# Optimization experiments

Measured on AMD Instinct MI355X. Metric: run time of the kernel, lower is better.

Reference implementation:

```python
import jax, jax.numpy as jnp
import numpy as np

BS, EMB, RES = 256, 768, 14
N_MASKS, HID, OUT, N_PROJ = 16, 4096, 256, 4
BN_EPS = 1e-5


def setup_inputs() -> dict:
    key = jax.random.key(0)
    ks = jax.random.split(key, 8)
    x = jax.random.normal(ks[0], (BS, EMB, RES, RES), jnp.float32)
    # binary ROI masks over the 14x14 = 196 patch grid
    masks = (jax.random.uniform(ks[1], (BS, N_MASKS, RES * RES)) < 0.3).astype(jnp.float32)
    projection_idx = jax.random.randint(ks[2], (N_MASKS,), 0, N_PROJ, jnp.int32)
    mask_ids = jax.random.randint(ks[3], (BS, N_MASKS), 0, 100, jnp.int32)
    # stacked params for the N_PROJ MLP projectors
    W1 = jax.random.normal(ks[4], (N_PROJ, EMB, HID), jnp.float32) * 0.02
    b1 = jnp.zeros((N_PROJ, HID), jnp.float32)
    gamma = jnp.ones((N_PROJ, HID), jnp.float32)
    beta = jnp.zeros((N_PROJ, HID), jnp.float32)
    W2 = jax.random.normal(ks[5], (N_PROJ, HID, OUT), jnp.float32) * 0.02
    b2 = jnp.zeros((N_PROJ, OUT), jnp.float32)
    return {"x": x, "masks": masks, "projection_idx": projection_idx,
            "mask_ids": mask_ids, "W1": W1, "b1": b1, "gamma": gamma,
            "beta": beta, "W2": W2, "b2": b2}


def reference(x, masks, projection_idx, mask_ids, W1, b1, gamma, beta, W2, b2):
    bs, emb, hx, hy = x.shape
    # [bs, emb, hx, hy] -> [bs, hw, emb]
    emb_local = jnp.transpose(x, (0, 2, 3, 1)).reshape(bs, hx * hy, emb)
    # mask-normalized pooling:  pooled[b,n,:] = mean of embeddings inside mask n
    area = masks.sum(axis=-1, keepdims=True)
    smpl = masks / jnp.maximum(area, 1.0)
    pooled = smpl @ emb_local                       # [bs, n_masks, emb]
    # dense dispatch: run EVERY projector over all pooled tokens (as original)
    h = jnp.einsum('bne,peh->pbnh', pooled, W1) + b1[:, None, None, :]
    # BatchNorm1d in training mode over flattened (bs*n_masks) batch, per projector
    mu = h.mean(axis=(1, 2), keepdims=True)
    var = jnp.mean(jnp.square(h - mu), axis=(1, 2), keepdims=True)  # biased var
    h = (h - mu) * jax.lax.rsqrt(var + BN_EPS) * gamma[:, None, None, :] + beta[:, None, None, :]
    h = jax.nn.relu(h)
    o = jnp.einsum('pbnh,pho->pbno', h, W2) + b2[:, None, None, :]   # [P, bs, n, out]
    # keep only projector projection_idx[n] for mask-slot n (disjoint selection)
    n_proj = W1.shape[0]
    sel = (projection_idx[None, :] == jnp.arange(n_proj)[:, None]).astype(o.dtype)  # [P, n]
    xs = (o * sel[:, None, :, None]).sum(axis=0)     # [bs, n_masks, out]
    return (xs, mask_ids)
```

## Files before the change

### kernel.cpp

```cpp
#include <hip/hip_runtime.h>
#include <hip/hip_bf16.h>

#define BS 256
#define EMB 768
#define HW 196
#define NMASK 16
#define HID 4096
#define OUT 256
#define NPROJ 4
#define MROWS 4096

typedef __attribute__((ext_vector_type(8))) short bf16x8;
typedef __attribute__((ext_vector_type(4))) float f32x4;
typedef __attribute__((ext_vector_type(8))) unsigned short u16x8;

__device__ inline float bf2f(unsigned short u) {
    unsigned int x = ((unsigned int)u) << 16;
    return __builtin_bit_cast(float, x);
}
__device__ inline short f2bfs(float f) {
    return __builtin_bit_cast(short, __float2bfloat16(f));
}

#define GL16(gptr, lptr)                                                     \
    __builtin_amdgcn_global_load_lds(                                        \
        (const __attribute__((address_space(1))) void*)(gptr),               \
        (__attribute__((address_space(3))) void*)(lptr), 16, 0, 0)

__global__ __launch_bounds__(256) void maskprep(
    const float* __restrict__ masks, short* __restrict__ afrG,
    float* __restrict__ invG)
{
    const int b = blockIdx.x, tid = threadIdx.x;
    const float* mb = masks + (size_t)b * NMASK * HW;
    short* ag = afrG + (size_t)b * 3584;
    for (int s = tid; s < 7 * 64; s += 256) {
        int m = s & 15, kb = ((s >> 4) & 3) * 8 + (s >> 6) * 32;
        bf16x8 v;
        #pragma unroll
        for (int j = 0; j < 8; ++j) {
            int kk = kb + j;
            v[j] = (kk < HW) ? f2bfs(mb[m * HW + kk]) : (short)0;
        }
        *(bf16x8*)(ag + s * 8) = v;
    }
    if (tid >= 192) {
        int l = tid - 192, m = l >> 2, q = l & 3;
        float a = 0.f;
        for (int hw = q; hw < HW; hw += 4) a += mb[m * HW + hw];
        a += __shfl_xor(a, 1);
        a += __shfl_xor(a, 2);
        if (q == 0) invG[b * NMASK + m] = 1.0f / fmaxf(a, 1.0f);
    }
}

__global__ __launch_bounds__(256) void pool_main(
    const float* __restrict__ x, const short* __restrict__ afrG,
    const float* __restrict__ invG, __hip_bfloat16* __restrict__ pooledG)
{
    __shared__ __align__(16) short afr[3584];
    __shared__ float inv[NMASK];
    const int bid = blockIdx.x;
    const int b = bid / 12, ec = bid % 12;
    const int tid = threadIdx.x, lane = tid & 63, w = tid >> 6;
    const int lc = lane & 15, l4 = lane >> 4;

    const int e = ec * 64 + w * 16 + lc;
    const float* xrow = x + ((size_t)b * EMB + e) * HW;
    float4 u[6][2];
    #pragma unroll
    for (int kc = 0; kc < 6; ++kc) {
        u[kc][0] = *(const float4*)(xrow + kc * 32 + l4 * 8);
        u[kc][1] = *(const float4*)(xrow + kc * 32 + l4 * 8 + 4);
    }
    float4 ut = (l4 == 0) ? *(const float4*)(xrow + 192)
                          : float4{0.f, 0.f, 0.f, 0.f};

    {
        const char* src = (const char*)(afrG + (size_t)b * 3584);
        #pragma unroll
        for (int r = 0; r < 2; ++r) {
            int cb = r * 256 + w * 64;
            if (cb < 448)
                GL16(src + (size_t)cb * 16 + (size_t)lane * 16,
                     (char*)afr + cb * 16);
        }
    }
    if (tid < NMASK) inv[tid] = invG[b * NMASK + tid];
    __syncthreads();

    const bf16x8* afv = (const bf16x8*)afr;
    f32x4 acc = {};
    #pragma unroll
    for (int kc = 0; kc < 6; ++kc) {
        bf16x8 af = afv[kc * 64 + lane];
        bf16x8 bf;
        bf[0] = f2bfs(u[kc][0].x); bf[1] = f2bfs(u[kc][0].y);
        bf[2] = f2bfs(u[kc][0].z); bf[3] = f2bfs(u[kc][0].w);
        bf[4] = f2bfs(u[kc][1].x); bf[5] = f2bfs(u[kc][1].y);
        bf[6] = f2bfs(u[kc][1].z); bf[7] = f2bfs(u[kc][1].w);
        acc = __builtin_amdgcn_mfma_f32_16x16x32_bf16(af, bf, acc, 0, 0, 0);
    }
    {
        bf16x8 af = afv[6 * 64 + lane];
        bf16x8 bf = {};
        if (l4 == 0) {
            bf[0] = f2bfs(ut.x); bf[1] = f2bfs(ut.y);
            bf[2] = f2bfs(ut.z); bf[3] = f2bfs(ut.w);
        }
        acc = __builtin_amdgcn_mfma_f32_16x16x32_bf16(af, bf, acc, 0, 0, 0);
    }

    #pragma unroll
    for (int j = 0; j < 4; ++j) {
        int m = l4 * 4 + j;
        pooledG[((size_t)m * 256 + b) * EMB + e] =
            __float2bfloat16(acc[j] * inv[m]);
    }
}

__global__ __launch_bounds__(256) void prep(
    const float* __restrict__ W1, const float* __restrict__ W2,
    const __hip_bfloat16* __restrict__ pg,
    __hip_bfloat16* __restrict__ W1T, __hip_bfloat16* __restrict__ W2T,
    __hip_bfloat16* __restrict__ pgT)
{
    __shared__ __align__(16) char sm[64 * 65 * 4];
    const int bid = blockIdx.x, tid = threadIdx.x;
    if (bid < 4096) {
        const float* src; __hip_bfloat16* dst; int R, C, x, y, z;
        if (bid < 3072) { z = bid / 768; int r = bid % 768; x = r % 64; y = r / 64;
                          src = W1; dst = W1T; R = EMB; C = HID; }
        else            { int b2 = bid - 3072; z = b2 / 256; int r = b2 % 256;
                          x = r % 4; y = r / 4; src = W2; dst = W2T; R = HID; C = OUT; }
        float (*tile)[65] = (float(*)[65])sm;
        const float* s = src + (size_t)z * R * C;
        __hip_bfloat16* d = dst + (size_t)z * R * C;
        const int c0 = x * 64, r0 = y * 64;
        for (int i = tid; i < 4096; i += 256) {
            int r = i >> 6, c = i & 63;
            tile[r][c] = s[(size_t)(r0 + r) * C + c0 + c];
        }
        __syncthreads();
        for (int i = tid; i < 4096; i += 256) {
            int c = i >> 6, r = i & 63;
            d[(size_t)(c0 + c) * R + r0 + r] = __float2bfloat16(tile[r][c]);
        }
    } else {
        const int b3 = bid - 4096;
        const int x = b3 % 12, y = b3 / 12;
        __hip_bfloat16 (*tile)[65] = (__hip_bfloat16(*)[65])sm;
        const int c0 = x * 64, r0 = y * 64;
        for (int i = tid; i < 4096; i += 256) {
            int r = i >> 6, c = i & 63;
            tile[r][c] = pg[(size_t)(r0 + r) * EMB + c0 + c];
        }
        __syncthreads();
        for (int i = tid; i < 4096; i += 256) {
            int c = i >> 6, r = i & 63;
            pgT[(size_t)(c0 + c) * MROWS + r0 + r] = tile[r][c];
        }
    }
}

__global__ __launch_bounds__(256) void meanpool(
    const __hip_bfloat16* __restrict__ PT, float* __restrict__ mp)
{
    const int e = blockIdx.x, tid = threadIdx.x;
    const u16x8* p = (const u16x8*)(PT + (size_t)e * MROWS);
    u16x8 v1 = p[tid], v2 = p[tid + 256];
    float s = 0.f;
    #pragma unroll
    for (int j = 0; j < 8; ++j) s += bf2f((unsigned short)v1[j]) + bf2f((unsigned short)v2[j]);
    #pragma unroll
    for (int o = 1; o < 64; o <<= 1) s += __shfl_xor(s, o);
    __shared__ float wsum[4];
    if ((tid & 63) == 0) wsum[tid >> 6] = s;
    __syncthreads();
    if (tid == 0) mp[e] = (wsum[0] + wsum[1] + wsum[2] + wsum[3]) * (1.0f / 4096.0f);
}

__global__ __launch_bounds__(256) void cgemm(
    const __hip_bfloat16* __restrict__ PT, float* __restrict__ Cpart)
{
    __shared__ __align__(16) __hip_bfloat16 As[128 * 32];
    __shared__ __align__(16) __hip_bfloat16 Bs[128 * 32];
    const int tid = threadIdx.x, lane = tid & 63, wid = tid >> 6;
    const int n0 = blockIdx.x * 128, m0 = blockIdx.y * 128, kbase = blockIdx.z * 512;
    float* Cp = Cpart + (size_t)blockIdx.z * EMB * EMB;
    const int wr = wid >> 1, wc = wid & 1;
    const int l4 = lane >> 4, lc = lane & 15;

    f32x4 acc[4][4] = {};
    for (int k0 = kbase; k0 < kbase + 512; k0 += 32) {
        __syncthreads();
        #pragma unroll
        for (int r = 0; r < 2; ++r) {
            int t = r * 256 + tid;
            int row = t >> 2, ko = (t & 3) * 8;
            GL16(PT + (size_t)(m0 + row) * MROWS + k0 + ko, &As[(r * 256 + wid * 64) * 8]);
        }
        #pragma unroll
        for (int r = 0; r < 2; ++r) {
            int t = r * 256 + tid;
            int row = t >> 2, ko = (t & 3) * 8;
            GL16(PT + (size_t)(n0 + row) * MROWS + k0 + ko, &Bs[(r * 256 + wid * 64) * 8]);
        }
        __syncthreads();
        const bf16x8* Av = (const bf16x8*)As;
        const bf16x8* Bv = (const bf16x8*)Bs;
        bf16x8 a[4], b[4];
        #pragma unroll
        for (int m = 0; m < 4; ++m) a[m] = Av[(wr * 64 + m * 16 + lc) * 4 + l4];
        #pragma unroll
        for (int n = 0; n < 4; ++n) b[n] = Bv[(wc * 64 + n * 16 + lc) * 4 + l4];
        #pragma unroll
        for (int m = 0; m < 4; ++m)
            #pragma unroll
            for (int n = 0; n < 4; ++n)
                acc[m][n] = __builtin_amdgcn_mfma_f32_16x16x32_bf16(a[m], b[n], acc[m][n], 0, 0, 0);
    }
    #pragma unroll
    for (int m = 0; m < 4; ++m)
        #pragma unroll
        for (int n = 0; n < 4; ++n)
            #pragma unroll
            for (int j = 0; j < 4; ++j) {
                int row = m0 + wr * 64 + m * 16 + l4 * 4 + j;
                int col = n0 + wc * 64 + n * 16 + lc;
                Cp[(size_t)row * EMB + col] = acc[m][n][j];
            }
}

__global__ __launch_bounds__(256) void cvt_c(
    const float* __restrict__ Cpart, __hip_bfloat16* __restrict__ Cbf)
{
    int i = (blockIdx.x * 256 + threadIdx.x) * 4;
    float sx = 0.f, sy = 0.f, sz = 0.f, sw = 0.f;
    #pragma unroll
    for (int kz = 0; kz < 8; ++kz) {
        float4 v = *(const float4*)(Cpart + (size_t)kz * EMB * EMB + i);
        sx += v.x; sy += v.y; sz += v.z; sw += v.w;
    }
    const float s = 1.0f / 4096.0f;
    Cbf[i + 0] = __float2bfloat16(sx * s);
    Cbf[i + 1] = __float2bfloat16(sy * s);
    Cbf[i + 2] = __float2bfloat16(sz * s);
    Cbf[i + 3] = __float2bfloat16(sw * s);
}

__global__ __launch_bounds__(256) void ugemm(
    const __hip_bfloat16* __restrict__ W1T, const __hip_bfloat16* __restrict__ Cbf,
    const float* __restrict__ mp,
    float* __restrict__ Eh2p, float* __restrict__ Mup)
{
    __shared__ __align__(16) __hip_bfloat16 As[128 * 32];
    __shared__ __align__(16) __hip_bfloat16 Bs[128 * 32];
    const int tid = threadIdx.x, lane = tid & 63, wid = tid >> 6;
    const int n0 = blockIdx.x * 128, m0 = blockIdx.y * 128, p = blockIdx.z;
    const __hip_bfloat16* Ap = W1T + (size_t)p * HID * EMB;
    const int wr = wid >> 1, wc = wid & 1;
    const int l4 = lane >> 4, lc = lane & 15;

    f32x4 acc[4][4] = {};
    for (int k0 = 0; k0 < EMB; k0 += 32) {
        __syncthreads();
        #pragma unroll
        for (int r = 0; r < 2; ++r) {
            int t = r * 256 + tid;
            int row = t >> 2, ko = (t & 3) * 8;
            GL16(Ap + (size_t)(m0 + row) * EMB + k0 + ko, &As[(r * 256 + wid * 64) * 8]);
        }
        #pragma unroll
        for (int r = 0; r < 2; ++r) {
            int t = r * 256 + tid;
            int row = t >> 2, ko = (t & 3) * 8;
            GL16(Cbf + (size_t)(n0 + row) * EMB + k0 + ko, &Bs[(r * 256 + wid * 64) * 8]);
        }
        __syncthreads();
        const bf16x8* Av = (const bf16x8*)As;
        const bf16x8* Bv = (const bf16x8*)Bs;
        bf16x8 a[4], b[4];
        #pragma unroll
        for (int m = 0; m < 4; ++m) a[m] = Av[(wr * 64 + m * 16 + lc) * 4 + l4];
        #pragma unroll
        for (int n = 0; n < 4; ++n) b[n] = Bv[(wc * 64 + n * 16 + lc) * 4 + l4];
        #pragma unroll
        for (int m = 0; m < 4; ++m)
            #pragma unroll
            for (int n = 0; n < 4; ++n)
                acc[m][n] = __builtin_amdgcn_mfma_f32_16x16x32_bf16(a[m], b[n], acc[m][n], 0, 0, 0);
    }

    float mpv[4];
    #pragma unroll
    for (int n = 0; n < 4; ++n) mpv[n] = mp[n0 + wc * 64 + n * 16 + lc];
    #pragma unroll
    for (int m = 0; m < 4; ++m) {
        #pragma unroll
        for (int j = 0; j < 4; ++j) {
            int row = m0 + wr * 64 + m * 16 + l4 * 4 + j;
            const __hip_bfloat16* wrow = Ap + (size_t)row * EMB;
            float e2 = 0.f, mu = 0.f;
            #pragma unroll
            for (int n = 0; n < 4; ++n) {
                int col = n0 + wc * 64 + n * 16 + lc;
                float wv = bf2f(__builtin_bit_cast(unsigned short, wrow[col]));
                e2 += acc[m][n][j] * wv;
                mu += mpv[n] * wv;
            }
            e2 += __shfl_xor(e2, 1); e2 += __shfl_xor(e2, 2);
            e2 += __shfl_xor(e2, 4); e2 += __shfl_xor(e2, 8);
            mu += __shfl_xor(mu, 1); mu += __shfl_xor(mu, 2);
            mu += __shfl_xor(mu, 4); mu += __shfl_xor(mu, 8);
            if (lc == 0) {
                size_t idx = (((size_t)blockIdx.x * 2 + wc) * NPROJ + p) * HID + row;
                Eh2p[idx] = e2;
                Mup [idx] = mu;
            }
        }
    }
}

__global__ __launch_bounds__(256) void finalize(
    const float* __restrict__ Eh2p, const float* __restrict__ Mup,
    const float* __restrict__ gamma, const float* __restrict__ beta,
    float* __restrict__ sbuf, float* __restrict__ tbuf)
{
    int i = blockIdx.x * 256 + threadIdx.x;
    float e2 = 0.f, mu = 0.f;
    #pragma unroll
    for (int bx = 0; bx < 12; ++bx) {
        e2 += Eh2p[bx * (NPROJ * HID) + i];
        mu += Mup [bx * (NPROJ * HID) + i];
    }
    float var = e2 - mu * mu;
    float is  = rsqrtf(fmaxf(var, 0.0f) + 1e-5f);
    float sc  = gamma[i] * is;
    sbuf[i] = sc;
    tbuf[i] = beta[i] - mu * sc;
}

__global__ __launch_bounds__(512, 2) void gemm1_sel(
    const __hip_bfloat16* __restrict__ A, const __hip_bfloat16* __restrict__ W1T,
    const int* __restrict__ proj,
    const float* __restrict__ sbuf, const float* __restrict__ tbuf,
    __hip_bfloat16* __restrict__ hrelu)
{
    __shared__ __align__(16) short LS[3 * 16384];
    const int tid = threadIdx.x, lane = tid & 63, w = tid >> 6;
    const int wr = w >> 2, wc = w & 3;
    const int lc = lane & 15, l4 = lane >> 4;
    const int n0 = blockIdx.x * 256, m0 = blockIdx.y * 256;
    const int p = proj[blockIdx.y];
    const __hip_bfloat16* Ag = A;
    const __hip_bfloat16* Bg = W1T + (size_t)p * HID * EMB;
    const bf16x8* LSv = (const bf16x8*)LS;

    auto STAGE = [&](int t) {
        const int sb = (t % 3) * 32768;
        #pragma unroll
        for (int ab = 0; ab < 2; ++ab) {
            const __hip_bfloat16* g = ab ? Bg : Ag;
            const int rbase = ab ? n0 : m0;
            #pragma unroll
            for (int i = 0; i < 2; ++i) {
                int c = (w * 2 + i) * 64 + lane;
                int row = c >> 2, ps = c & 3;
                int ls = ps ^ (row & 3);
                const __hip_bfloat16* src =
                    g + (size_t)(rbase + row) * EMB + t * 32 + ls * 8;
                GL16(src, (char*)LS + sb + ab * 16384 + (w * 2 + i) * 1024);
            }
        }
    };

    f32x4 acc[8][4] = {};

    STAGE(0);
    STAGE(1);
    asm volatile("s_waitcnt vmcnt(4)" ::: "memory");
    __builtin_amdgcn_s_barrier();

    for (int t = 0; t < 24; ++t) {
        if (t + 2 < 24) STAGE(t + 2);
        const int vb = (t % 3) * 2048;

        bf16x8 bfr[4];
        #pragma unroll
        for (int nf = 0; nf < 4; ++nf) {
            int rb = wc * 64 + nf * 16 + lc;
            bfr[nf] = LSv[vb + 1024 + rb * 4 + (l4 ^ (rb & 3))];
        }
        #pragma unroll
        for (int q = 0; q < 4; ++q) {
            bf16x8 afr[2];
            #pragma unroll
            for (int m2 = 0; m2 < 2; ++m2) {
                int ra = wr * 128 + (q * 2 + m2) * 16 + lc;
                afr[m2] = LSv[vb + ra * 4 + (l4 ^ (ra & 3))];
            }
            __builtin_amdgcn_s_setprio(1);
            #pragma unroll
            for (int m2 = 0; m2 < 2; ++m2)
                #pragma unroll
                for (int nf = 0; nf < 4; ++nf)
                    acc[q * 2 + m2][nf] = __builtin_amdgcn_mfma_f32_16x16x32_bf16(
                        afr[m2], bfr[nf], acc[q * 2 + m2][nf], 0, 0, 0);
            __builtin_amdgcn_s_setprio(0);
        }

        if (t + 2 < 24) {
            asm volatile("s_waitcnt vmcnt(4)" ::: "memory");
            __builtin_amdgcn_s_barrier();
        } else if (t + 2 == 24) {
            asm volatile("s_waitcnt vmcnt(0)" ::: "memory");
            __builtin_amdgcn_s_barrier();
        }
    }

    #pragma unroll
    for (int nf = 0; nf < 4; ++nf) {
        int col = n0 + wc * 64 + nf * 16 + lc;
        float s = sbuf[p * HID + col];
        float tt = tbuf[p * HID + col];
        #pragma unroll
        for (int mf = 0; mf < 8; ++mf)
            #pragma unroll
            for (int j = 0; j < 4; ++j) {
                int row = m0 + wr * 128 + mf * 16 + l4 * 4 + j;
                float v = fmaxf(acc[mf][nf][j] * s + tt, 0.0f);
                hrelu[(size_t)row * HID + col] = __float2bfloat16(v);
            }
    }
}

__global__ __launch_bounds__(256) void gemm2(
    const __hip_bfloat16* __restrict__ Hn, const __hip_bfloat16* __restrict__ W2T,
    const int* __restrict__ proj, float* __restrict__ Opart)
{
    __shared__ __align__(16) __hip_bfloat16 As[128 * 32];
    __shared__ __align__(16) __hip_bfloat16 Bs[128 * 32];
    const int tid = threadIdx.x, lane = tid & 63, wid = tid >> 6;
    const int nmask = blockIdx.x;
    const int bc    = blockIdx.y;
    const int ct    = blockIdx.z >> 2, kz = blockIdx.z & 3;
    const int p = proj[nmask];
    const __hip_bfloat16* Ap = Hn + (size_t)(nmask * 256 + bc * 128) * HID;
    const __hip_bfloat16* Bp = W2T + ((size_t)p * OUT + ct * 128) * HID;
    float* Op = Opart + (size_t)kz * MROWS * OUT;
    const int wr = wid >> 1, wc = wid & 1;
    const int l4 = lane >> 4, lc = lane & 15;

    f32x4 acc[4][4] = {};
    for (int k0 = kz * 1024; k0 < kz * 1024 + 1024; k0 += 32) {
        __syncthreads();
        #pragma unroll
        for (int r = 0; r < 2; ++r) {
            int t = r * 256 + tid;
            int row = t >> 2, ko = (t & 3) * 8;
            GL16(Ap + (size_t)row * HID + k0 + ko, &As[(r * 256 + wid * 64) * 8]);
        }
        #pragma unroll
        for (int r = 0; r < 2; ++r) {
            int t = r * 256 + tid;
            int row = t >> 2, ko = (t & 3) * 8;
            GL16(Bp + (size_t)row * HID + k0 + ko, &Bs[(r * 256 + wid * 64) * 8]);
        }
        __syncthreads();
        const bf16x8* Av = (const bf16x8*)As;
        const bf16x8* Bv = (const bf16x8*)Bs;
        bf16x8 a[4], b[4];
        #pragma unroll
        for (int m = 0; m < 4; ++m) a[m] = Av[(wr * 64 + m * 16 + lc) * 4 + l4];
        #pragma unroll
        for (int n = 0; n < 4; ++n) b[n] = Bv[(wc * 64 + n * 16 + lc) * 4 + l4];
        #pragma unroll
        for (int m = 0; m < 4; ++m)
            #pragma unroll
            for (int n = 0; n < 4; ++n)
                acc[m][n] = __builtin_amdgcn_mfma_f32_16x16x32_bf16(a[m], b[n], acc[m][n], 0, 0, 0);
    }

    #pragma unroll
    for (int m = 0; m < 4; ++m)
        #pragma unroll
        for (int n = 0; n < 4; ++n)
            #pragma unroll
            for (int j = 0; j < 4; ++j) {
                int bb = bc * 128 + wr * 64 + m * 16 + l4 * 4 + j;
                int oc = ct * 128 + wc * 64 + n * 16 + lc;
                Op[((size_t)bb * NMASK + nmask) * OUT + oc] = acc[m][n][j];
            }
}

__global__ __launch_bounds__(256) void reduce_out(
    const float* __restrict__ Opart, const float* __restrict__ b2,
    const int* __restrict__ proj, const int* __restrict__ mids,
    float* __restrict__ out)
{
    int i = (blockIdx.x * 256 + threadIdx.x) * 4;
    float sx = 0.f, sy = 0.f, sz = 0.f, sw = 0.f;
    #pragma unroll
    for (int kz = 0; kz < 4; ++kz) {
        float4 v = *(const float4*)(Opart + (size_t)kz * MROWS * OUT + i);
        sx += v.x; sy += v.y; sz += v.z; sw += v.w;
    }
    int nm = (i >> 8) & 15;
    int p  = proj[nm];
    float4 bv = *(const float4*)(b2 + p * OUT + (i & 255));
    float4 r;
    r.x = sx + bv.x; r.y = sy + bv.y; r.z = sz + bv.z; r.w = sw + bv.w;
    *(float4*)(out + i) = r;
    if (blockIdx.x < 16) {
        int t = blockIdx.x * 256 + threadIdx.x;
        out[(size_t)MROWS * OUT + t] = (float)mids[t];
    }
}

extern "C" void kernel_launch(void* const* d_in, const int* in_sizes, int n_in,
                              void* d_out, int out_size, void* d_ws, size_t ws_size,
                              hipStream_t stream)
{
    const float* x     = (const float*)d_in[0];
    const float* masks = (const float*)d_in[1];
    const int*   proj  = (const int*)d_in[2];
    const int*   mids  = (const int*)d_in[3];
    const float* W1    = (const float*)d_in[4];
    const float* gamma = (const float*)d_in[6];
    const float* beta  = (const float*)d_in[7];
    const float* W2    = (const float*)d_in[8];
    const float* b2    = (const float*)d_in[9];
    float* out = (float*)d_out;

    char* ws = (char*)d_ws;
    __hip_bfloat16* pooledG = (__hip_bfloat16*)(ws);
    __hip_bfloat16* W1T     = (__hip_bfloat16*)(ws + 6291456);
    __hip_bfloat16* W2T     = (__hip_bfloat16*)(ws + 31457280);
    float*          mp      = (float*)(ws + 39845888);
    float*          Eh2p    = (float*)(ws + 39848960);
    float*          Mup     = (float*)(ws + 40635392);
    float*          sbuf    = (float*)(ws + 41421824);
    float*          tbuf    = (float*)(ws + 41487360);
    short*          afrG    = (short*)(ws + 41552896);
    float*          invG    = (float*)(ws + 43387904);
    char* R = ws + 43404288;
    __hip_bfloat16* pooledT = (__hip_bfloat16*)(R);
    float*          Cpart   = (float*)(R + 6291456);
    __hip_bfloat16* Cbf     = (__hip_bfloat16*)(R + 25165824);
    __hip_bfloat16* hrelu   = (__hip_bfloat16*)(R);
    float*          Opart   = (float*)(R + 33554432);

    maskprep<<<BS, 256, 0, stream>>>(masks, afrG, invG);
    pool_main<<<3072, 256, 0, stream>>>(x, afrG, invG, pooledG);
    prep<<<4864, 256, 0, stream>>>(W1, W2, pooledG, W1T, W2T, pooledT);
    meanpool<<<EMB, 256, 0, stream>>>(pooledT, mp);
    cgemm<<<dim3(6, 6, 8), 256, 0, stream>>>(pooledT, Cpart);
    cvt_c<<<(EMB * EMB) / 1024, 256, 0, stream>>>(Cpart, Cbf);
    ugemm<<<dim3(6, 32, 4), 256, 0, stream>>>(W1T, Cbf, mp, Eh2p, Mup);
    finalize<<<(NPROJ * HID) / 256, 256, 0, stream>>>(Eh2p, Mup, gamma, beta, sbuf, tbuf);
    gemm1_sel<<<dim3(HID / 256, MROWS / 256), 512, 0, stream>>>(pooledG, W1T, proj, sbuf, tbuf, hrelu);
    gemm2<<<dim3(NMASK, 2, 8), 256, 0, stream>>>(hrelu, W2T, proj, Opart);
    reduce_out<<<(MROWS * OUT) / 1024, 256, 0, stream>>>(Opart, b2, proj, mids, out);
}
```

Baseline: 194.4 us.

## Fuse pooling with weight transposes, compute mean in pooling epilogue

```diff
diff --git a/kernel.cpp b/kernel.cpp
--- a/kernel.cpp
+++ b/kernel.cpp
@@ -54,89 +54,90 @@
     }
 }
 
-__global__ __launch_bounds__(256) void pool_main(
+__global__ __launch_bounds__(256) void fused2(
     const float* __restrict__ x, const short* __restrict__ afrG,
-    const float* __restrict__ invG, __hip_bfloat16* __restrict__ pooledG)
-{
-    __shared__ __align__(16) short afr[3584];
-    __shared__ float inv[NMASK];
-    const int bid = blockIdx.x;
-    const int b = bid / 12, ec = bid % 12;
-    const int tid = threadIdx.x, lane = tid & 63, w = tid >> 6;
-    const int lc = lane & 15, l4 = lane >> 4;
-
-    const int e = ec * 64 + w * 16 + lc;
-    const float* xrow = x + ((size_t)b * EMB + e) * HW;
-    float4 u[6][2];
-    #pragma unroll
-    for (int kc = 0; kc < 6; ++kc) {
-        u[kc][0] = *(const float4*)(xrow + kc * 32 + l4 * 8);
-        u[kc][1] = *(const float4*)(xrow + kc * 32 + l4 * 8 + 4);
-    }
-    float4 ut = (l4 == 0) ? *(const float4*)(xrow + 192)
-                          : float4{0.f, 0.f, 0.f, 0.f};
-
-    {
-        const char* src = (const char*)(afrG + (size_t)b * 3584);
-        #pragma unroll
-        for (int r = 0; r < 2; ++r) {
-            int cb = r * 256 + w * 64;
-            if (cb < 448)
-                GL16(src + (size_t)cb * 16 + (size_t)lane * 16,
-                     (char*)afr + cb * 16);
-        }
-    }
-    if (tid < NMASK) inv[tid] = invG[b * NMASK + tid];
-    __syncthreads();
-
-    const bf16x8* afv = (const bf16x8*)afr;
-    f32x4 acc = {};
-    #pragma unroll
-    for (int kc = 0; kc < 6; ++kc) {
-        bf16x8 af = afv[kc * 64 + lane];
-        bf16x8 bf;
-        bf[0] = f2bfs(u[kc][0].x); bf[1] = f2bfs(u[kc][0].y);
-        bf[2] = f2bfs(u[kc][0].z); bf[3] = f2bfs(u[kc][0].w);
-        bf[4] = f2bfs(u[kc][1].x); bf[5] = f2bfs(u[kc][1].y);
-        bf[6] = f2bfs(u[kc][1].z); bf[7] = f2bfs(u[kc][1].w);
-        acc = __builtin_amdgcn_mfma_f32_16x16x32_bf16(af, bf, acc, 0, 0, 0);
-    }
-    {
-        bf16x8 af = afv[6 * 64 + lane];
-        bf16x8 bf = {};
-        if (l4 == 0) {
-            bf[0] = f2bfs(ut.x); bf[1] = f2bfs(ut.y);
-            bf[2] = f2bfs(ut.z); bf[3] = f2bfs(ut.w);
-        }
-        acc = __builtin_amdgcn_mfma_f32_16x16x32_bf16(af, bf, acc, 0, 0, 0);
-    }
-
-    #pragma unroll
-    for (int j = 0; j < 4; ++j) {
-        int m = l4 * 4 + j;
-        pooledG[((size_t)m * 256 + b) * EMB + e] =
-            __float2bfloat16(acc[j] * inv[m]);
-    }
-}
-
-__global__ __launch_bounds__(256) void prep(
+    const float* __restrict__ invG,
     const float* __restrict__ W1, const float* __restrict__ W2,
-    const __hip_bfloat16* __restrict__ pg,
-    __hip_bfloat16* __restrict__ W1T, __hip_bfloat16* __restrict__ W2T,
-    __hip_bfloat16* __restrict__ pgT)
-{
-    __shared__ __align__(16) char sm[64 * 65 * 4];
+    __hip_bfloat16* __restrict__ pooledG, float* __restrict__ mpB,
+    __hip_bfloat16* __restrict__ W1T, __hip_bfloat16* __restrict__ W2T)
+{
+    __shared__ __align__(16) char smu[16704];
     const int bid = blockIdx.x, tid = threadIdx.x;
-    if (bid < 4096) {
-        const float* src; __hip_bfloat16* dst; int R, C, x, y, z;
-        if (bid < 3072) { z = bid / 768; int r = bid % 768; x = r % 64; y = r / 64;
-                          src = W1; dst = W1T; R = EMB; C = HID; }
-        else            { int b2 = bid - 3072; z = b2 / 256; int r = b2 % 256;
-                          x = r % 4; y = r / 4; src = W2; dst = W2T; R = HID; C = OUT; }
-        float (*tile)[65] = (float(*)[65])sm;
+
+    if (bid < 3072) {
+        short* afr = (short*)smu;
+        float* inv = (float*)(smu + 14592);
+        const int b = bid / 12, ec = bid % 12;
+        const int lane = tid & 63, w = tid >> 6;
+        const int lc = lane & 15, l4 = lane >> 4;
+
+        const int e = ec * 64 + w * 16 + lc;
+        const float* xrow = x + ((size_t)b * EMB + e) * HW;
+        float4 u[6][2];
+        #pragma unroll
+        for (int kc = 0; kc < 6; ++kc) {
+            u[kc][0] = *(const float4*)(xrow + kc * 32 + l4 * 8);
+            u[kc][1] = *(const float4*)(xrow + kc * 32 + l4 * 8 + 4);
+        }
+        float4 ut = (l4 == 0) ? *(const float4*)(xrow + 192)
+                              : float4{0.f, 0.f, 0.f, 0.f};
+
+        {
+            const char* src = (const char*)(afrG + (size_t)b * 3584);
+            #pragma unroll
+            for (int r = 0; r < 2; ++r) {
+                int cb = r * 256 + w * 64;
+                if (cb < 448)
+                    GL16(src + (size_t)cb * 16 + (size_t)lane * 16,
+                         (char*)afr + cb * 16);
+            }
+        }
+        if (tid < NMASK) inv[tid] = invG[b * NMASK + tid];
+        __syncthreads();
+
+        const bf16x8* afv = (const bf16x8*)afr;
+        f32x4 acc = {};
+        #pragma unroll
+        for (int kc = 0; kc < 6; ++kc) {
+            bf16x8 af = afv[kc * 64 + lane];
+            bf16x8 bf;
+            bf[0] = f2bfs(u[kc][0].x); bf[1] = f2bfs(u[kc][0].y);
+            bf[2] = f2bfs(u[kc][0].z); bf[3] = f2bfs(u[kc][0].w);
+            bf[4] = f2bfs(u[kc][1].x); bf[5] = f2bfs(u[kc][1].y);
+            bf[6] = f2bfs(u[kc][1].z); bf[7] = f2bfs(u[kc][1].w);
+            acc = __builtin_amdgcn_mfma_f32_16x16x32_bf16(af, bf, acc, 0, 0, 0);
+        }
+        {
+            bf16x8 af = afv[6 * 64 + lane];
+            bf16x8 bf = {};
+            if (l4 == 0) {
+                bf[0] = f2bfs(ut.x); bf[1] = f2bfs(ut.y);
+                bf[2] = f2bfs(ut.z); bf[3] = f2bfs(ut.w);
+            }
+            acc = __builtin_amdgcn_mfma_f32_16x16x32_bf16(af, bf, acc, 0, 0, 0);
+        }
+
+        float msum = 0.f;
+        #pragma unroll
+        for (int j = 0; j < 4; ++j) {
+            int m = l4 * 4 + j;
+            float v = acc[j] * inv[m];
+            msum += v;
+            pooledG[((size_t)m * 256 + b) * EMB + e] = __float2bfloat16(v);
+        }
+        msum += __shfl_xor(msum, 16);
+        msum += __shfl_xor(msum, 32);
+        if (l4 == 0) mpB[(size_t)b * EMB + e] = msum;
+    } else {
+        const float* src; __hip_bfloat16* dst; int R, C, xx, yy, z;
+        if (bid < 6144) { int idx = bid - 3072; z = idx / 768; int r = idx % 768;
+                          xx = r % 64; yy = r / 64; src = W1; dst = W1T; R = EMB; C = HID; }
+        else            { int idx = bid - 6144; z = idx / 256; int r = idx % 256;
+                          xx = r % 4;  yy = r / 4;  src = W2; dst = W2T; R = HID; C = OUT; }
+        float (*tile)[65] = (float(*)[65])smu;
         const float* s = src + (size_t)z * R * C;
         __hip_bfloat16* d = dst + (size_t)z * R * C;
-        const int c0 = x * 64, r0 = y * 64;
+        const int c0 = xx * 64, r0 = yy * 64;
         for (int i = tid; i < 4096; i += 256) {
             int r = i >> 6, c = i & 63;
             tile[r][c] = s[(size_t)(r0 + r) * C + c0 + c];
@@ -146,38 +147,23 @@
             int c = i >> 6, r = i & 63;
             d[(size_t)(c0 + c) * R + r0 + r] = __float2bfloat16(tile[r][c]);
         }
-    } else {
-        const int b3 = bid - 4096;
-        const int x = b3 % 12, y = b3 / 12;
-        __hip_bfloat16 (*tile)[65] = (__hip_bfloat16(*)[65])sm;
-        const int c0 = x * 64, r0 = y * 64;
-        for (int i = tid; i < 4096; i += 256) {
-            int r = i >> 6, c = i & 63;
-            tile[r][c] = pg[(size_t)(r0 + r) * EMB + c0 + c];
-        }
-        __syncthreads();
-        for (int i = tid; i < 4096; i += 256) {
-            int c = i >> 6, r = i & 63;
-            pgT[(size_t)(c0 + c) * MROWS + r0 + r] = tile[r][c];
-        }
-    }
-}
-
-__global__ __launch_bounds__(256) void meanpool(
-    const __hip_bfloat16* __restrict__ PT, float* __restrict__ mp)
-{
-    const int e = blockIdx.x, tid = threadIdx.x;
-    const u16x8* p = (const u16x8*)(PT + (size_t)e * MROWS);
-    u16x8 v1 = p[tid], v2 = p[tid + 256];
-    float s = 0.f;
-    #pragma unroll
-    for (int j = 0; j < 8; ++j) s += bf2f((unsigned short)v1[j]) + bf2f((unsigned short)v2[j]);
-    #pragma unroll
-    for (int o = 1; o < 64; o <<= 1) s += __shfl_xor(s, o);
-    __shared__ float wsum[4];
-    if ((tid & 63) == 0) wsum[tid >> 6] = s;
+    }
+}
+
+__global__ __launch_bounds__(256) void pgT_kernel(
+    const __hip_bfloat16* __restrict__ src, __hip_bfloat16* __restrict__ dst)
+{
+    __shared__ __hip_bfloat16 tile[64][65];
+    const int c0 = blockIdx.x * 64, r0 = blockIdx.y * 64, tid = threadIdx.x;
+    for (int i = tid; i < 4096; i += 256) {
+        int r = i >> 6, c = i & 63;
+        tile[r][c] = src[(size_t)(r0 + r) * EMB + c0 + c];
+    }
     __syncthreads();
-    if (tid == 0) mp[e] = (wsum[0] + wsum[1] + wsum[2] + wsum[3]) * (1.0f / 4096.0f);
+    for (int i = tid; i < 4096; i += 256) {
+        int c = i >> 6, r = i & 63;
+        dst[(size_t)(c0 + c) * MROWS + r0 + r] = tile[r][c];
+    }
 }
 
 __global__ __launch_bounds__(256) void cgemm(
@@ -233,20 +219,29 @@
 }
 
 __global__ __launch_bounds__(256) void cvt_c(
-    const float* __restrict__ Cpart, __hip_bfloat16* __restrict__ Cbf)
-{
-    int i = (blockIdx.x * 256 + threadIdx.x) * 4;
-    float sx = 0.f, sy = 0.f, sz = 0.f, sw = 0.f;
-    #pragma unroll
-    for (int kz = 0; kz < 8; ++kz) {
-        float4 v = *(const float4*)(Cpart + (size_t)kz * EMB * EMB + i);
-        sx += v.x; sy += v.y; sz += v.z; sw += v.w;
-    }
-    const float s = 1.0f / 4096.0f;
-    Cbf[i + 0] = __float2bfloat16(sx * s);
-    Cbf[i + 1] = __float2bfloat16(sy * s);
-    Cbf[i + 2] = __float2bfloat16(sz * s);
-    Cbf[i + 3] = __float2bfloat16(sw * s);
+    const float* __restrict__ Cpart, const float* __restrict__ mpB,
+    __hip_bfloat16* __restrict__ Cbf, float* __restrict__ mp)
+{
+    const int bid = blockIdx.x, tid = threadIdx.x;
+    if (bid < 576) {
+        int i = (bid * 256 + tid) * 4;
+        float sx = 0.f, sy = 0.f, sz = 0.f, sw = 0.f;
+        #pragma unroll
+        for (int kz = 0; kz < 8; ++kz) {
+            float4 v = *(const float4*)(Cpart + (size_t)kz * EMB * EMB + i);
+            sx += v.x; sy += v.y; sz += v.z; sw += v.w;
+        }
+        const float s = 1.0f / 4096.0f;
+        Cbf[i + 0] = __float2bfloat16(sx * s);
+        Cbf[i + 1] = __float2bfloat16(sy * s);
+        Cbf[i + 2] = __float2bfloat16(sz * s);
+        Cbf[i + 3] = __float2bfloat16(sw * s);
+    } else {
+        int e = (bid - 576) * 256 + tid;
+        float s = 0.f;
+        for (int b = 0; b < 256; ++b) s += mpB[(size_t)b * EMB + e];
+        mp[e] = s * (1.0f / 4096.0f);
+    }
 }
 
 __global__ __launch_bounds__(256) void ugemm(
@@ -544,7 +539,8 @@
     float*          tbuf    = (float*)(ws + 41487360);
     short*          afrG    = (short*)(ws + 41552896);
     float*          invG    = (float*)(ws + 43387904);
-    char* R = ws + 43404288;
+    float*          mpB     = (float*)(ws + 43404288);
+    char* R = ws + 44190720;
     __hip_bfloat16* pooledT = (__hip_bfloat16*)(R);
     float*          Cpart   = (float*)(R + 6291456);
     __hip_bfloat16* Cbf     = (__hip_bfloat16*)(R + 25165824);
@@ -552,11 +548,10 @@
     float*          Opart   = (float*)(R + 33554432);
 
     maskprep<<<BS, 256, 0, stream>>>(masks, afrG, invG);
-    pool_main<<<3072, 256, 0, stream>>>(x, afrG, invG, pooledG);
-    prep<<<4864, 256, 0, stream>>>(W1, W2, pooledG, W1T, W2T, pooledT);
-    meanpool<<<EMB, 256, 0, stream>>>(pooledT, mp);
+    fused2<<<7168, 256, 0, stream>>>(x, afrG, invG, W1, W2, pooledG, mpB, W1T, W2T);
+    pgT_kernel<<<dim3(EMB / 64, MROWS / 64), 256, 0, stream>>>(pooledG, pooledT);
     cgemm<<<dim3(6, 6, 8), 256, 0, stream>>>(pooledT, Cpart);
-    cvt_c<<<(EMB * EMB) / 1024, 256, 0, stream>>>(Cpart, Cbf);
+    cvt_c<<<579, 256, 0, stream>>>(Cpart, mpB, Cbf, mp);
     ugemm<<<dim3(6, 32, 4), 256, 0, stream>>>(W1T, Cbf, mp, Eh2p, Mup);
     finalize<<<(NPROJ * HID) / 256, 256, 0, stream>>>(Eh2p, Mup, gamma, beta, sbuf, tbuf);
     gemm1_sel<<<dim3(HID / 256, MROWS / 256), 512, 0, stream>>>(pooledG, W1T, proj, sbuf, tbuf, hrelu);
```

Result: slower. 199.4 us (+2.6%).
